# Kernel tuning notes

Measured on AMD Instinct MI355X. Metric: run time of the kernel, lower is better.

## Reference

```python
import jax, jax.numpy as jnp
import numpy as np

EPS = 1e-12  # torch F.normalize default eps


def _l2_normalize(x):
    # normalize along last dim, matching F.normalize(dim=2)
    norm = jnp.linalg.norm(x, axis=-1, keepdims=True)
    return x / jnp.maximum(norm, EPS)


def _poly_kernel_mean(a, b):
    # mean over (B,C,C) of squared inner products along T.
    # Original does broadcast (B,1,C,T)*(B,C,1,T) then sum; einsum is the
    # efficient batched-matmul form of the same math.
    g = jnp.einsum('bct,bdt->bcd', a, b)  # (B,C,C)
    return jnp.mean(g * g)


def setup_inputs() -> dict:
    key = jax.random.key(0)
    k1, k2 = jax.random.split(key)
    B, C, T = 16, 128, 16384
    f_s = jax.random.normal(k1, (B, C, T), dtype=jnp.float32)
    f_t = jax.random.normal(k2, (B, C, T), dtype=jnp.float32)
    return {"f_s": f_s, "f_t": f_t}


def reference(f_s, f_t):
    # equal T -> no interpolation branch; view(B,C,-1) is identity for 3D
    s = _l2_normalize(f_s)
    t = _l2_normalize(f_t)
    loss = (jax.lax.stop_gradient(_poly_kernel_mean(t, t))
            + _poly_kernel_mean(s, s)
            - 2.0 * _poly_kernel_mean(s, t))
    return loss
```

## Files before the change

### kernel.cpp

```cpp
#include <hip/hip_runtime.h>
#include <hip/hip_bf16.h>

#define BATCH  16
#define CCH    128
#define TDIM   16384
#define MROWS  256
#define NCHUNK 16
#define KC     (TDIM / NCHUNK)
#define BK     32
#define NSTEP  (KC / BK)
#define LDSP   40
#define GRAM   (MROWS * MROWS)

typedef __attribute__((ext_vector_type(8))) short bf16x8;
typedef __attribute__((ext_vector_type(4))) float f32x4;
typedef __attribute__((ext_vector_type(4))) unsigned short u16x4;

__device__ __forceinline__ unsigned short f2bf(float x) {
  unsigned int u = __float_as_uint(x);
  u += 0x7fffu + ((u >> 16) & 1u);
  return (unsigned short)(u >> 16);
}

__global__ __launch_bounds__(512, 2) void gram_kernel(
    const float* __restrict__ fs, const float* __restrict__ ft,
    float* __restrict__ outp, int atomic_mode)
{
  __shared__ __attribute__((aligned(16))) unsigned short sm[2][MROWS][LDSP];

  const int tid   = threadIdx.x;
  const int bidx  = blockIdx.x;
  const int b     = bidx / NCHUNK;
  const int chunk = bidx - b * NCHUNK;
  const int kbase = chunk * KC;

  const int lane = tid & 63;
  const int w    = tid >> 6;
  const int wr   = w & 3;
  const int wc   = w >> 2;
  const int lhi  = lane >> 4;
  const int llo  = lane & 15;
  const int koff = lhi * 8;

  const float* rowptr[4];
  int rowidx[4], kq4[4];
  #pragma unroll
  for (int j = 0; j < 4; ++j) {
    int idx = j * 512 + tid;
    int row = idx >> 3;
    int kq  = idx & 7;
    rowidx[j] = row;
    kq4[j]    = kq * 4;
    const float* base = (row < CCH)
        ? (fs + (size_t)(b * CCH + row) * TDIM)
        : (ft + (size_t)(b * CCH + (row - CCH)) * TDIM);
    rowptr[j] = base + kbase + kq * 4;
  }

  f32x4 acc[4][8];
  #pragma unroll
  for (int i = 0; i < 4; ++i)
    #pragma unroll
    for (int j = 0; j < 8; ++j)
      acc[i][j] = (f32x4){0.f, 0.f, 0.f, 0.f};

  #pragma unroll
  for (int j = 0; j < 4; ++j) {
    f32x4 v = *(const f32x4*)(rowptr[j]);
    u16x4 p;
    p.x = f2bf(v.x); p.y = f2bf(v.y); p.z = f2bf(v.z); p.w = f2bf(v.w);
    *(u16x4*)&sm[0][rowidx[j]][kq4[j]] = p;
  }
  __syncthreads();

  int cur = 0;
  #pragma unroll 1
  for (int s = 0; s < NSTEP - 1; ++s) {
    f32x4 v[4];
    #pragma unroll
    for (int j = 0; j < 4; ++j)
      v[j] = *(const f32x4*)(rowptr[j] + (s + 1) * BK);

    bf16x8 af[4], bfr[8];
    #pragma unroll
    for (int i = 0; i < 4; ++i)
      af[i] = *(const bf16x8*)&sm[cur][wr * 64 + i * 16 + llo][koff];
    #pragma unroll
    for (int j = 0; j < 8; ++j)
      bfr[j] = *(const bf16x8*)&sm[cur][wc * 128 + j * 16 + llo][koff];
    #pragma unroll
    for (int i = 0; i < 4; ++i)
      #pragma unroll
      for (int j = 0; j < 8; ++j)
        acc[i][j] = __builtin_amdgcn_mfma_f32_16x16x32_bf16(af[i], bfr[j], acc[i][j], 0, 0, 0);

    #pragma unroll
    for (int j = 0; j < 4; ++j) {
      u16x4 p;
      p.x = f2bf(v[j].x); p.y = f2bf(v[j].y); p.z = f2bf(v[j].z); p.w = f2bf(v[j].w);
      *(u16x4*)&sm[cur ^ 1][rowidx[j]][kq4[j]] = p;
    }
    __syncthreads();
    cur ^= 1;
  }

  {
    bf16x8 af[4], bfr[8];
    #pragma unroll
    for (int i = 0; i < 4; ++i)
      af[i] = *(const bf16x8*)&sm[cur][wr * 64 + i * 16 + llo][koff];
    #pragma unroll
    for (int j = 0; j < 8; ++j)
      bfr[j] = *(const bf16x8*)&sm[cur][wc * 128 + j * 16 + llo][koff];
    #pragma unroll
    for (int i = 0; i < 4; ++i)
      #pragma unroll
      for (int j = 0; j < 8; ++j)
        acc[i][j] = __builtin_amdgcn_mfma_f32_16x16x32_bf16(af[i], bfr[j], acc[i][j], 0, 0, 0);
  }

  if (atomic_mode) {
    float* out = outp + (size_t)b * GRAM;
    #pragma unroll
    for (int i = 0; i < 4; ++i) {
      int row0 = wr * 64 + i * 16 + lhi * 4;
      #pragma unroll
      for (int j = 0; j < 8; ++j) {
        int col = wc * 128 + j * 16 + llo;
        #pragma unroll
        for (int r = 0; r < 4; ++r)
          atomicAdd(&out[(size_t)(row0 + r) * MROWS + col], acc[i][j][r]);
      }
    }
  } else {
    float* out = outp + (size_t)bidx * GRAM;
    #pragma unroll
    for (int i = 0; i < 4; ++i) {
      int row0 = wr * 64 + i * 16 + lhi * 4;
      #pragma unroll
      for (int j = 0; j < 8; ++j) {
        int col = wc * 128 + j * 16 + llo;
        #pragma unroll
        for (int r = 0; r < 4; ++r)
          out[(size_t)(row0 + r) * MROWS + col] = acc[i][j][r];
      }
    }
  }
}

__global__ __launch_bounds__(256) void norms_kernel(
    const float* __restrict__ gram, float* __restrict__ norms, int nchunk)
{
  int b = blockIdx.x;
  int d = threadIdx.x;
  float g = 0.f;
  for (int c = 0; c < nchunk; ++c)
    g += gram[(size_t)(b * nchunk + c) * GRAM + (size_t)d * (MROWS + 1)];
  float n = sqrtf(fmaxf(g, 0.f));
  n = fmaxf(n, 1e-12f);
  norms[b * MROWS + d] = 1.0f / n;
}

__global__ __launch_bounds__(256) void loss_kernel(
    const float* __restrict__ gram, const float* __restrict__ norms,
    float* __restrict__ out, int nchunk)
{
  int b     = blockIdx.x >> 6;
  int strip = blockIdx.x & 63;
  int e0    = strip * 1024 + threadIdx.x * 4;
  const float* nb = norms + b * MROWS;

  f32x4 g = (f32x4){0.f, 0.f, 0.f, 0.f};
  for (int c = 0; c < nchunk; ++c) {
    f32x4 v = *(const f32x4*)(gram + (size_t)(b * nchunk + c) * GRAM + e0);
    g.x += v.x; g.y += v.y; g.z += v.z; g.w += v.w;
  }
  int i  = e0 >> 8;
  int j0 = e0 & 255;
  float ri = nb[i];
  float accl = 0.f;
  #pragma unroll
  for (int q = 0; q < 4; ++q) {
    int j = j0 + q;
    float gh = g[q] * ri * nb[j];
    float sgn = ((i < CCH) == (j < CCH)) ? 1.f : -1.f;
    accl += sgn * gh * gh;
  }
  #pragma unroll
  for (int off = 32; off > 0; off >>= 1)
    accl += __shfl_down(accl, off, 64);
  __shared__ float red[4];
  if ((threadIdx.x & 63) == 0) red[threadIdx.x >> 6] = accl;
  __syncthreads();
  if (threadIdx.x == 0) {
    float t = red[0] + red[1] + red[2] + red[3];
    atomicAdd(out, t * (1.0f / (float)(BATCH * CCH * CCH)));
  }
}

extern "C" void kernel_launch(void* const* d_in, const int* in_sizes, int n_in,
                              void* d_out, int out_size, void* d_ws, size_t ws_size,
                              hipStream_t stream) {
  const float* fs = (const float*)d_in[0];
  const float* ft = (const float*)d_in[1];
  float* out = (float*)d_out;
  float* wsf = (float*)d_ws;

  float* norms = wsf;
  float* gram  = wsf + 4096;

  const size_t need_partials = (size_t)(4096 + (size_t)BATCH * NCHUNK * GRAM) * 4;
  const int atomic_mode = (ws_size >= need_partials) ? 0 : 1;
  const int nchunk = atomic_mode ? 1 : NCHUNK;

  (void)hipMemsetAsync(d_out, 0, sizeof(float), stream);
  if (atomic_mode)
    (void)hipMemsetAsync(gram, 0, (size_t)BATCH * GRAM * sizeof(float), stream);

  gram_kernel<<<dim3(BATCH * NCHUNK), dim3(512), 0, stream>>>(fs, ft, gram, atomic_mode);
  norms_kernel<<<dim3(BATCH), dim3(256), 0, stream>>>(gram, norms, nchunk);
  loss_kernel<<<dim3(BATCH * 64), dim3(256), 0, stream>>>(gram, norms, out, nchunk);
}
```

Measured before the change: 323.3 us.

## Deepen global prefetch to two steps, widen LDS stores, separate diagonal partials

The gram kernel now gives each thread half a row (16 floats) and stores to LDS with 16-byte writes. It prefetches global data two K-steps ahead into a register ring instead of one, which hides more memory latency at the cost of extra registers under the 2-blocks launch bound. The diagonal of each partial Gram is written to a small separate buffer, so the norms kernel no longer reads strided values from the large partial array. The loss kernel gets vectorized norm loads and simpler indexing.

```diff
diff --git a/kernel.cpp b/kernel.cpp
--- a/kernel.cpp
+++ b/kernel.cpp
@@ -12,9 +12,13 @@
 #define LDSP   40
 #define GRAM   (MROWS * MROWS)
 
+#define WS_NORMS 0
+#define WS_DIAG  4096
+#define WS_BODY  (4096 + 65536)
+
 typedef __attribute__((ext_vector_type(8))) short bf16x8;
 typedef __attribute__((ext_vector_type(4))) float f32x4;
-typedef __attribute__((ext_vector_type(4))) unsigned short u16x4;
+typedef __attribute__((ext_vector_type(8))) unsigned short u16x8;
 
 __device__ __forceinline__ unsigned short f2bf(float x) {
   unsigned int u = __float_as_uint(x);
@@ -24,7 +28,7 @@
 
 __global__ __launch_bounds__(512, 2) void gram_kernel(
     const float* __restrict__ fs, const float* __restrict__ ft,
-    float* __restrict__ outp, int atomic_mode)
+    float* __restrict__ outp, float* __restrict__ diagp, int atomic_mode)
 {
   __shared__ __attribute__((aligned(16))) unsigned short sm[2][MROWS][LDSP];
 
@@ -42,20 +46,12 @@
   const int llo  = lane & 15;
   const int koff = lhi * 8;
 
-  const float* rowptr[4];
-  int rowidx[4], kq4[4];
-  #pragma unroll
-  for (int j = 0; j < 4; ++j) {
-    int idx = j * 512 + tid;
-    int row = idx >> 3;
-    int kq  = idx & 7;
-    rowidx[j] = row;
-    kq4[j]    = kq * 4;
-    const float* base = (row < CCH)
-        ? (fs + (size_t)(b * CCH + row) * TDIM)
-        : (ft + (size_t)(b * CCH + (row - CCH)) * TDIM);
-    rowptr[j] = base + kbase + kq * 4;
-  }
+  const int srow = tid >> 1;
+  const int half = tid & 1;
+  const float* rp = ((srow < CCH)
+      ? (fs + (size_t)(b * CCH + srow) * TDIM)
+      : (ft + (size_t)(b * CCH + (srow - CCH)) * TDIM))
+      + kbase + half * 16;
 
   f32x4 acc[4][8];
   #pragma unroll
@@ -64,59 +60,57 @@
     for (int j = 0; j < 8; ++j)
       acc[i][j] = (f32x4){0.f, 0.f, 0.f, 0.f};
 
-  #pragma unroll
-  for (int j = 0; j < 4; ++j) {
-    f32x4 v = *(const f32x4*)(rowptr[j]);
-    u16x4 p;
-    p.x = f2bf(v.x); p.y = f2bf(v.y); p.z = f2bf(v.z); p.w = f2bf(v.w);
-    *(u16x4*)&sm[0][rowidx[j]][kq4[j]] = p;
-  }
+  {
+    f32x4 v0 = *(const f32x4*)(rp + 0);
+    f32x4 v1 = *(const f32x4*)(rp + 4);
+    f32x4 v2 = *(const f32x4*)(rp + 8);
+    f32x4 v3 = *(const f32x4*)(rp + 12);
+    u16x8 pa, pb;
+    pa[0]=f2bf(v0.x); pa[1]=f2bf(v0.y); pa[2]=f2bf(v0.z); pa[3]=f2bf(v0.w);
+    pa[4]=f2bf(v1.x); pa[5]=f2bf(v1.y); pa[6]=f2bf(v1.z); pa[7]=f2bf(v1.w);
+    pb[0]=f2bf(v2.x); pb[1]=f2bf(v2.y); pb[2]=f2bf(v2.z); pb[3]=f2bf(v2.w);
+    pb[4]=f2bf(v3.x); pb[5]=f2bf(v3.y); pb[6]=f2bf(v3.z); pb[7]=f2bf(v3.w);
+    *(u16x8*)&sm[0][srow][half * 16]     = pa;
+    *(u16x8*)&sm[0][srow][half * 16 + 8] = pb;
+  }
+  f32x4 p[2][4];
+  #pragma unroll
+  for (int k = 0; k < 4; ++k)
+    p[1][k] = *(const f32x4*)(rp + 1 * BK + k * 4);
   __syncthreads();
 
-  int cur = 0;
-  #pragma unroll 1
-  for (int s = 0; s < NSTEP - 1; ++s) {
-    f32x4 v[4];
-    #pragma unroll
-    for (int j = 0; j < 4; ++j)
-      v[j] = *(const f32x4*)(rowptr[j] + (s + 1) * BK);
-
-    bf16x8 af[4], bfr[8];
-    #pragma unroll
-    for (int i = 0; i < 4; ++i)
-      af[i] = *(const bf16x8*)&sm[cur][wr * 64 + i * 16 + llo][koff];
-    #pragma unroll
-    for (int j = 0; j < 8; ++j)
-      bfr[j] = *(const bf16x8*)&sm[cur][wc * 128 + j * 16 + llo][koff];
-    #pragma unroll
-    for (int i = 0; i < 4; ++i)
+  #pragma unroll 2
+  for (int s = 0; s < NSTEP; ++s) {
+    const int par = s & 1;
+    if (s + 2 < NSTEP) {
+      #pragma unroll
+      for (int k = 0; k < 4; ++k)
+        p[par][k] = *(const f32x4*)(rp + (s + 2) * BK + k * 4);
+    }
+    {
+      bf16x8 af[4], bfr[8];
+      #pragma unroll
+      for (int i = 0; i < 4; ++i)
+        af[i] = *(const bf16x8*)&sm[par][wr * 64 + i * 16 + llo][koff];
       #pragma unroll
       for (int j = 0; j < 8; ++j)
-        acc[i][j] = __builtin_amdgcn_mfma_f32_16x16x32_bf16(af[i], bfr[j], acc[i][j], 0, 0, 0);
-
-    #pragma unroll
-    for (int j = 0; j < 4; ++j) {
-      u16x4 p;
-      p.x = f2bf(v[j].x); p.y = f2bf(v[j].y); p.z = f2bf(v[j].z); p.w = f2bf(v[j].w);
-      *(u16x4*)&sm[cur ^ 1][rowidx[j]][kq4[j]] = p;
+        bfr[j] = *(const bf16x8*)&sm[par][wc * 128 + j * 16 + llo][koff];
+      #pragma unroll
+      for (int i = 0; i < 4; ++i)
+        #pragma unroll
+        for (int j = 0; j < 8; ++j)
+          acc[i][j] = __builtin_amdgcn_mfma_f32_16x16x32_bf16(af[i], bfr[j], acc[i][j], 0, 0, 0);
+    }
+    if (s + 1 < NSTEP) {
+      u16x8 pa, pb;
+      pa[0]=f2bf(p[par^1][0].x); pa[1]=f2bf(p[par^1][0].y); pa[2]=f2bf(p[par^1][0].z); pa[3]=f2bf(p[par^1][0].w);
+      pa[4]=f2bf(p[par^1][1].x); pa[5]=f2bf(p[par^1][1].y); pa[6]=f2bf(p[par^1][1].z); pa[7]=f2bf(p[par^1][1].w);
+      pb[0]=f2bf(p[par^1][2].x); pb[1]=f2bf(p[par^1][2].y); pb[2]=f2bf(p[par^1][2].z); pb[3]=f2bf(p[par^1][2].w);
+      pb[4]=f2bf(p[par^1][3].x); pb[5]=f2bf(p[par^1][3].y); pb[6]=f2bf(p[par^1][3].z); pb[7]=f2bf(p[par^1][3].w);
+      *(u16x8*)&sm[par ^ 1][srow][half * 16]     = pa;
+      *(u16x8*)&sm[par ^ 1][srow][half * 16 + 8] = pb;
     }
     __syncthreads();
-    cur ^= 1;
-  }
-
-  {
-    bf16x8 af[4], bfr[8];
-    #pragma unroll
-    for (int i = 0; i < 4; ++i)
-      af[i] = *(const bf16x8*)&sm[cur][wr * 64 + i * 16 + llo][koff];
-    #pragma unroll
-    for (int j = 0; j < 8; ++j)
-      bfr[j] = *(const bf16x8*)&sm[cur][wc * 128 + j * 16 + llo][koff];
-    #pragma unroll
-    for (int i = 0; i < 4; ++i)
-      #pragma unroll
-      for (int j = 0; j < 8; ++j)
-        acc[i][j] = __builtin_amdgcn_mfma_f32_16x16x32_bf16(af[i], bfr[j], acc[i][j], 0, 0, 0);
   }
 
   if (atomic_mode) {
@@ -132,6 +126,13 @@
           atomicAdd(&out[(size_t)(row0 + r) * MROWS + col], acc[i][j][r]);
       }
     }
+    if ((wr >> 1) == wc && (llo >> 2) == lhi) {
+      #pragma unroll
+      for (int i = 0; i < 4; ++i) {
+        float dv = (wr & 1) ? acc[i][4 + i][llo & 3] : acc[i][i][llo & 3];
+        atomicAdd(&diagp[b * MROWS + wr * 64 + i * 16 + llo], dv);
+      }
+    }
   } else {
     float* out = outp + (size_t)bidx * GRAM;
     #pragma unroll
@@ -145,45 +146,56 @@
           out[(size_t)(row0 + r) * MROWS + col] = acc[i][j][r];
       }
     }
+    if ((wr >> 1) == wc && (llo >> 2) == lhi) {
+      #pragma unroll
+      for (int i = 0; i < 4; ++i) {
+        float dv = (wr & 1) ? acc[i][4 + i][llo & 3] : acc[i][i][llo & 3];
+        diagp[bidx * MROWS + wr * 64 + i * 16 + llo] = dv;
+      }
+    }
   }
 }
 
 __global__ __launch_bounds__(256) void norms_kernel(
-    const float* __restrict__ gram, float* __restrict__ norms, int nchunk)
+    const float* __restrict__ diagp, float* __restrict__ norms, int nchunk)
 {
   int b = blockIdx.x;
   int d = threadIdx.x;
   float g = 0.f;
   for (int c = 0; c < nchunk; ++c)
-    g += gram[(size_t)(b * nchunk + c) * GRAM + (size_t)d * (MROWS + 1)];
+    g += diagp[(b * nchunk + c) * MROWS + d];
   float n = sqrtf(fmaxf(g, 0.f));
   n = fmaxf(n, 1e-12f);
   norms[b * MROWS + d] = 1.0f / n;
 }
 
 __global__ __launch_bounds__(256) void loss_kernel(
-    const float* __restrict__ gram, const float* __restrict__ norms,
+    const float* __restrict__ body, const float* __restrict__ norms,
     float* __restrict__ out, int nchunk)
 {
-  int b     = blockIdx.x >> 6;
-  int strip = blockIdx.x & 63;
-  int e0    = strip * 1024 + threadIdx.x * 4;
+  int flat = blockIdx.x * 1024 + threadIdx.x * 4;
+  int b    = flat >> 16;
+  int e    = flat & 65535;
   const float* nb = norms + b * MROWS;
 
   f32x4 g = (f32x4){0.f, 0.f, 0.f, 0.f};
+  const float* src = body + (size_t)b * nchunk * GRAM + e;
+  #pragma unroll 4
   for (int c = 0; c < nchunk; ++c) {
-    f32x4 v = *(const f32x4*)(gram + (size_t)(b * nchunk + c) * GRAM + e0);
+    f32x4 v = *(const f32x4*)(src + (size_t)c * GRAM);
     g.x += v.x; g.y += v.y; g.z += v.z; g.w += v.w;
   }
-  int i  = e0 >> 8;
-  int j0 = e0 & 255;
+  int i  = e >> 8;
+  int j0 = e & 255;
   float ri = nb[i];
+  f32x4 rj = *(const f32x4*)(nb + j0);
+  float si = (i < CCH) ? 1.f : -1.f;
   float accl = 0.f;
   #pragma unroll
   for (int q = 0; q < 4; ++q) {
     int j = j0 + q;
-    float gh = g[q] * ri * nb[j];
-    float sgn = ((i < CCH) == (j < CCH)) ? 1.f : -1.f;
+    float gh = g[q] * ri * rj[q];
+    float sgn = ((j < CCH) ? 1.f : -1.f) * si;
     accl += sgn * gh * gh;
   }
   #pragma unroll
@@ -203,21 +215,24 @@
                               hipStream_t stream) {
   const float* fs = (const float*)d_in[0];
   const float* ft = (const float*)d_in[1];
-  float* out = (float*)d_out;
-  float* wsf = (float*)d_ws;
-
-  float* norms = wsf;
-  float* gram  = wsf + 4096;
-
-  const size_t need_partials = (size_t)(4096 + (size_t)BATCH * NCHUNK * GRAM) * 4;
+  float* out   = (float*)d_out;
+  float* wsf   = (float*)d_ws;
+  float* norms = wsf + WS_NORMS;
+  float* diagp = wsf + WS_DIAG;
+  float* body  = wsf + WS_BODY;
+
+  const size_t need_partials =
+      (size_t)(WS_BODY + (size_t)BATCH * NCHUNK * GRAM) * sizeof(float);
   const int atomic_mode = (ws_size >= need_partials) ? 0 : 1;
   const int nchunk = atomic_mode ? 1 : NCHUNK;
 
   (void)hipMemsetAsync(d_out, 0, sizeof(float), stream);
-  if (atomic_mode)
-    (void)hipMemsetAsync(gram, 0, (size_t)BATCH * GRAM * sizeof(float), stream);
-
-  gram_kernel<<<dim3(BATCH * NCHUNK), dim3(512), 0, stream>>>(fs, ft, gram, atomic_mode);
-  norms_kernel<<<dim3(BATCH), dim3(256), 0, stream>>>(gram, norms, nchunk);
-  loss_kernel<<<dim3(BATCH * 64), dim3(256), 0, stream>>>(gram, norms, out, nchunk);
-}
+  if (atomic_mode) {
+    (void)hipMemsetAsync(diagp, 0,
+        (size_t)(65536 + (size_t)BATCH * GRAM) * sizeof(float), stream);
+  }
+
+  gram_kernel<<<dim3(BATCH * NCHUNK), dim3(512), 0, stream>>>(fs, ft, body, diagp, atomic_mode);
+  norms_kernel<<<dim3(BATCH), dim3(256), 0, stream>>>(diagp, norms, nchunk);
+  loss_kernel<<<dim3(1024), dim3(256), 0, stream>>>(body, norms, out, nchunk);
+}
```

New measurement: 332.4 us. +2.8%, slower.
